# Optimization experiments

Measured on AMD Instinct MI355X. Metric: run time of the kernel, lower is better.

The kernel has to match this reference:

```python
import jax, jax.numpy as jnp
import numpy as np

B, L, D, H = 8, 512, 512, 8
E, G = 4, 2            # primary experts, ghost experts
THRESH = 0.01          # ghost_activation_threshold
EPS = 1e-5             # LayerNorm eps (torch default)


def _ln(x, s, b):
    m = x.mean(-1, keepdims=True)
    v = ((x - m) ** 2).mean(-1, keepdims=True)
    return (x - m) * jax.lax.rsqrt(v + EPS) * s + b


def _expert(x, ln1_s, ln1_b, wqkv, bqkv, wo, bo, ln2_s, ln2_b, w1, b1, w2, b2):
    # Pre-norm transformer block: MHA + residual, FFN + residual (dropout=0)
    Bn, Ln, Dn = x.shape
    dh = Dn // H
    xn = _ln(x, ln1_s, ln1_b)
    qkv = xn @ wqkv + bqkv                      # [B,L,3D]
    q, k, v = jnp.split(qkv, 3, axis=-1)
    heads = lambda t: t.reshape(Bn, Ln, H, dh).transpose(0, 2, 1, 3)
    q, k, v = heads(q), heads(k), heads(v)      # [B,H,L,dh]
    scores = jnp.einsum('bhqd,bhkd->bhqk', q, k) / np.sqrt(dh).astype(np.float32)
    attn = jax.nn.softmax(scores, axis=-1)
    o = jnp.einsum('bhqk,bhkd->bhqd', attn, v).transpose(0, 2, 1, 3).reshape(Bn, Ln, Dn)
    x = x + o @ wo + bo
    h = _ln(x, ln2_s, ln2_b)
    x = x + jax.nn.gelu(h @ w1 + b1) @ w2 + b2
    return x


def _make_params(key, n, d):
    ks = jax.random.split(key, 4)
    s = 0.02
    return dict(
        ln1_s=jnp.ones((n, d)), ln1_b=jnp.zeros((n, d)),
        wqkv=jax.random.normal(ks[0], (n, d, 3 * d)) * s, bqkv=jnp.zeros((n, 3 * d)),
        wo=jax.random.normal(ks[1], (n, d, d)) * s, bo=jnp.zeros((n, d)),
        ln2_s=jnp.ones((n, d)), ln2_b=jnp.zeros((n, d)),
        w1=jax.random.normal(ks[2], (n, d, 4 * d)) * s, b1=jnp.zeros((n, 4 * d)),
        w2=jax.random.normal(ks[3], (n, 4 * d, d)) * s, b2=jnp.zeros((n, d)))


def setup_inputs() -> dict:
    key = jax.random.key(0)
    k1, k2, k3 = jax.random.split(key, 3)
    inp = {'x': jax.random.normal(k1, (B, L, D), jnp.float32), 'step': 100}
    for pre, n, k in (('p_', E, k2), ('g_', G, k3)):
        for name, arr in _make_params(k, n, D).items():
            inp[pre + name] = arr
    return inp


def reference(x, step,
              p_ln1_s, p_ln1_b, p_wqkv, p_bqkv, p_wo, p_bo, p_ln2_s, p_ln2_b, p_w1, p_b1, p_w2, p_b2,
              g_ln1_s, g_ln1_b, g_wqkv, g_bqkv, g_wo, g_bo, g_ln2_s, g_ln2_b, g_w1, g_b1, g_w2, g_b2):
    pp = (p_ln1_s, p_ln1_b, p_wqkv, p_bqkv, p_wo, p_bo, p_ln2_s, p_ln2_b, p_w1, p_b1, p_w2, p_b2)
    gp = (g_ln1_s, g_ln1_b, g_wqkv, g_bqkv, g_wo, g_bo, g_ln2_s, g_ln2_b, g_w1, g_b1, g_w2, g_b2)
    run = jax.vmap(lambda ps: _expert(x, *ps))
    prim = run(pp)                               # [E,B,L,D]
    # --- saturation metrics (statistics only; detached like .item() in torch) ---
    mean_eo = prim.mean(axis=(1, 2))             # [E,D]
    nrm = mean_eo / jnp.linalg.norm(mean_eo, axis=1, keepdims=True)
    gram = nrm @ nrm.T                           # [E,E]
    ortho = 1.0 - jnp.mean((gram - jnp.eye(E, dtype=gram.dtype)) ** 2)
    recon = prim.mean(axis=0)                    # [B,L,D]
    uvar = jnp.var(x - recon, ddof=1)            # torch.var unbiased default
    sat = jax.lax.stop_gradient(ortho * uvar)
    # --- ghost activation (initial state: all dormant -> ghost 0 gets 0.01) ---
    base = jnp.zeros((G,), x.dtype).at[0].set(0.01)
    rates = jnp.where(sat > THRESH, base, jnp.zeros((G,), x.dtype))
    ghost = jax.vmap(lambda ps: _expert(x, *ps))(gp) * rates[:, None, None, None]  # [G,B,L,D]
    # combine: mean over all (primary + ghost) expert outputs
    out = jnp.concatenate([prim, ghost], axis=0).mean(axis=0)  # [B,L,D]
    return out
```

## Files before the change

kernel.cpp:

```cpp
#include <hip/hip_runtime.h>

typedef __bf16 bf16;
typedef __bf16 bf16x8 __attribute__((ext_vector_type(8)));
typedef float  f32x4  __attribute__((ext_vector_type(4)));
typedef float  f32x16 __attribute__((ext_vector_type(16)));

#define AS1 __attribute__((address_space(1)))
#define AS3 __attribute__((address_space(3)))

__device__ __forceinline__ void async16(const void* g, void* l) {
  __builtin_amdgcn_global_load_lds((const AS1 unsigned int*)g, (AS3 unsigned int*)l, 16, 0, 0);
}

__device__ __forceinline__ float gelu_fast(float u) {
  float z = 0.7978845608028654f * (u + 0.044715f * u * u * u);
  z = fminf(fmaxf(z, -15.f), 15.f);
  float t = __expf(2.f * z);
  return u * t / (t + 1.f);
}

template <int FOLD>
__global__ __launch_bounds__(256) void transpose_cvt(
    const float* pbase, const float* gbase, bf16* dst, int K, int M,
    const float* lnsP, const float* lnbP, const float* lnsG, const float* lnbG,
    const float* b0P, const float* b0G, float* bias_eff) {
  __shared__ float tile[32][33];
  const int z = blockIdx.z;
  const float* src = (z < 4) ? pbase + (size_t)z * K * M : gbase;
  bf16* d = dst + (size_t)z * M * K;
  const int mBlk = blockIdx.x * 32, kBlk = blockIdx.y * 32;
  const int tx = threadIdx.x, ty = threadIdx.y;
  for (int i = 0; i < 4; i++)
    tile[ty + i * 8][tx] = src[(size_t)(kBlk + ty + i * 8) * M + mBlk + tx];
  __syncthreads();
  if constexpr (FOLD) {
    const float* s  = (z < 4) ? lnsP + (size_t)z * 512 : lnsG;
    const float* bb = (z < 4) ? lnbP + (size_t)z * 512 : lnbG;
    const float sk = s[kBlk + tx];
    for (int i = 0; i < 4; i++)
      d[(size_t)(mBlk + ty + i * 8) * K + kBlk + tx] = (bf16)(tile[tx][ty + i * 8] * sk);
    if (ty == 0) {
      float acc = 0.f;
      for (int kk = 0; kk < 32; kk++) acc += bb[kBlk + kk] * tile[kk][tx];
      if (kBlk == 0) {
        const float* b0 = (z < 4) ? b0P + (size_t)z * M : b0G;
        acc += b0[mBlk + tx];
      }
      atomicAdd(&bias_eff[(size_t)z * M + mBlk + tx], acc);
    }
  } else {
    for (int i = 0; i < 4; i++)
      d[(size_t)(mBlk + ty + i * 8) * K + kBlk + tx] = (bf16)tile[tx][ty + i * 8];
  }
}

__global__ __launch_bounds__(256) void ln_plain(const float* x, bf16* out) {
  const int t = blockIdx.x, tid = threadIdx.x;
  const float* xr = x + (size_t)t * 512;
  float v0 = xr[tid], v1 = xr[tid + 256];
  float s1 = v0 + v1, s2 = v0 * v0 + v1 * v1;
  for (int off = 32; off > 0; off >>= 1) { s1 += __shfl_down(s1, off); s2 += __shfl_down(s2, off); }
  __shared__ float red[8];
  __shared__ float mv[2];
  if ((tid & 63) == 0) { red[tid >> 6] = s1; red[4 + (tid >> 6)] = s2; }
  __syncthreads();
  if (tid == 0) {
    float a = red[0] + red[1] + red[2] + red[3];
    float b = red[4] + red[5] + red[6] + red[7];
    float mean = a * (1.f / 512.f);
    float var = b * (1.f / 512.f) - mean * mean;
    mv[0] = mean; mv[1] = 1.f / sqrtf(var + 1e-5f);
  }
  __syncthreads();
  const float mean = mv[0], rs = mv[1];
  bf16* o = out + (size_t)t * 512;
  o[tid]       = (bf16)((v0 - mean) * rs);
  o[tid + 256] = (bf16)((v1 - mean) * rs);
}

__global__ __launch_bounds__(256) void ln2_kernel(const bf16* in, const float* sP, const float* bP,
                                                  const float* sG, const float* bG, bf16* out) {
  const int t = blockIdx.x, z = blockIdx.y, tid = threadIdx.x;
  const bf16* xr = in + (size_t)z * 4096 * 512 + (size_t)t * 512;
  float v0 = (float)xr[tid], v1 = (float)xr[tid + 256];
  float s1 = v0 + v1, s2 = v0 * v0 + v1 * v1;
  for (int off = 32; off > 0; off >>= 1) { s1 += __shfl_down(s1, off); s2 += __shfl_down(s2, off); }
  __shared__ float red[8];
  __shared__ float mv[2];
  if ((tid & 63) == 0) { red[tid >> 6] = s1; red[4 + (tid >> 6)] = s2; }
  __syncthreads();
  if (tid == 0) {
    float a = red[0] + red[1] + red[2] + red[3];
    float b = red[4] + red[5] + red[6] + red[7];
    float mean = a * (1.f / 512.f);
    float var = b * (1.f / 512.f) - mean * mean;
    mv[0] = mean; mv[1] = 1.f / sqrtf(var + 1e-5f);
  }
  __syncthreads();
  const float mean = mv[0], rs = mv[1];
  const float* sc = (z < 4) ? sP + (size_t)z * 512 : sG;
  const float* bi = (z < 4) ? bP + (size_t)z * 512 : bG;
  bf16* o = out + (size_t)z * 4096 * 512 + (size_t)t * 512;
  o[tid]       = (bf16)((v0 - mean) * rs * sc[tid] + bi[tid]);
  o[tid + 256] = (bf16)((v1 - mean) * rs * sc[tid + 256] + bi[tid + 256]);
}

template <int MODE>
__global__ __launch_bounds__(256, 4) void gemm_bt(
    const bf16* Abase, long long aStrideZ, const bf16* Wt,
    const float* biasP, const float* biasG, int K, int M,
    bf16* out, const void* resid, long long residStrideZ) {
  const int bx = blockIdx.x, by = blockIdx.y, z = blockIdx.z;
  const bf16* A = Abase + (size_t)z * aStrideZ;
  const bf16* B = Wt + (size_t)z * M * K;
  const float* bias = (z < 4) ? biasP + (size_t)z * M : biasG;
  __shared__ bf16 smem[128 * 136];
  bf16* As = smem;
  bf16* Bs = smem + 128 * 64;
  const int tid = threadIdx.x, wave = tid >> 6, l = tid & 63;
  const int l31 = l & 31, lh = l >> 5;
  const int wm = wave & 1, wn = wave >> 1;
  f32x16 acc[2][2];
  for (int i = 0; i < 2; i++) for (int j = 0; j < 2; j++)
    for (int r = 0; r < 16; r++) acc[i][j][r] = 0.f;
  const int rowA0 = by * 128, rowB0 = bx * 128;

  for (int kt = 0; kt < K; kt += 64) {
    __syncthreads();
    for (int i = 0; i < 4; i++) {
      int s = i * 256 + tid, r = s >> 3, kb = s & 7;
      int swz = (r ^ (r >> 3)) & 7;
      int col = kt + ((kb ^ swz) << 3);
      async16(A + (size_t)(rowA0 + r) * K + col, &As[(i * 256 + wave * 64) * 8]);
      async16(B + (size_t)(rowB0 + r) * K + col, &Bs[(i * 256 + wave * 64) * 8]);
    }
    __syncthreads();
    for (int ks = 0; ks < 4; ks++) {
      bf16x8 af[2], bfr[2];
      for (int ti = 0; ti < 2; ti++) {
        int r = wm * 64 + ti * 32 + l31;
        int kb = (ks * 2 + lh) ^ ((r ^ (r >> 3)) & 7);
        af[ti] = *(const bf16x8*)&As[r * 64 + (kb << 3)];
      }
      for (int ni = 0; ni < 2; ni++) {
        int r = wn * 64 + ni * 32 + l31;
        int kb = (ks * 2 + lh) ^ ((r ^ (r >> 3)) & 7);
        bfr[ni] = *(const bf16x8*)&Bs[r * 64 + (kb << 3)];
      }
      for (int ti = 0; ti < 2; ti++)
        for (int ni = 0; ni < 2; ni++)
          acc[ti][ni] = __builtin_amdgcn_mfma_f32_32x32x16_bf16(af[ti], bfr[ni], acc[ti][ni], 0, 0, 0);
    }
  }

  __syncthreads();
  for (int ti = 0; ti < 2; ti++)
    for (int ni = 0; ni < 2; ni++) {
      int coll = wn * 64 + ni * 32 + l31;
      float bb = bias[rowB0 + coll];
      for (int reg = 0; reg < 16; reg++) {
        int row = wm * 64 + ti * 32 + (reg & 3) + 8 * (reg >> 2) + 4 * lh;
        float v = acc[ti][ni][reg] + bb;
        if constexpr (MODE == 2) v = gelu_fast(v);
        smem[row * 136 + coll] = (bf16)v;
      }
    }
  __syncthreads();
  bf16* ob = out + (size_t)z * 4096 * M;
  for (int p = 0; p < 8; p++) {
    int r = p * 16 + (tid >> 4), c0 = (tid & 15) * 8;
    bf16x8 vv = *(const bf16x8*)&smem[r * 136 + c0];
    if constexpr (MODE == 1) {
      const float* rx = (const float*)resid + (size_t)(rowA0 + r) * 512 + rowB0 + c0;
      for (int j = 0; j < 8; j++) vv[j] = (bf16)((float)vv[j] + rx[j]);
    } else if constexpr (MODE == 3) {
      const bf16* rx = (const bf16*)resid + (size_t)z * residStrideZ + (size_t)(rowA0 + r) * 512 + rowB0 + c0;
      bf16x8 rv = *(const bf16x8*)rx;
      for (int j = 0; j < 8; j++) vv[j] = (bf16)((float)vv[j] + (float)rv[j]);
    }
    *(bf16x8*)&ob[(size_t)(rowA0 + r) * M + rowB0 + c0] = vv;
  }
}

__global__ __launch_bounds__(256, 2) void attn_kernel(const bf16* qkv, bf16* o) {
  const int qt = blockIdx.x >> 6, bh = blockIdx.x & 63, z = blockIdx.y;
  const int b = bh >> 3, h = bh & 7;
  const bf16* base = qkv + (size_t)z * 4096 * 1536 + (size_t)b * 512 * 1536;
  __shared__ bf16 smem[30208];
  bf16* Vt = smem + 16384;
  bf16* Q_area = smem + 16384;
  const int tid = threadIdx.x, wave = tid >> 6, l = tid & 63;
  const int m16 = l & 15, q4 = l >> 4;
  bf16* pw = smem + 20992 + wave * 32 * 72;
  f32x4 zero4 = {0.f, 0.f, 0.f, 0.f};

  for (int i = 0; i < 4; i++) {
    int s = i * 256 + tid, r = s >> 3, kb = s & 7;
    async16(base + (size_t)(qt * 128 + r) * 1536 + h * 64 + ((kb ^ (r & 7)) << 3),
            &Q_area[(i * 256 + wave * 64) * 8]);
  }
  for (int i = 0; i < 2; i++) {
    int s = i * 256 + tid, r = s >> 3, kb = s & 7;
    async16(base + (size_t)r * 1536 + 512 + h * 64 + ((kb ^ (r & 7)) << 3),
            &smem[(i * 256 + wave * 64) * 8]);
    async16(base + (size_t)r * 1536 + 1024 + h * 64 + (kb << 3),
            &smem[8192 + (i * 256 + wave * 64) * 8]);
  }
  f32x4 Oacc[2][4];
  float l_run[2][4];
  for (int rt = 0; rt < 2; rt++)
    for (int cr = 0; cr < 4; cr++) l_run[rt][cr] = 0.f;
  for (int rt = 0; rt < 2; rt++) for (int dt = 0; dt < 4; dt++) Oacc[rt][dt] = zero4;
  __syncthreads();
  bf16x8 qf[2][2];
  for (int rt = 0; rt < 2; rt++)
    for (int ks = 0; ks < 2; ks++) {
      int r = wave * 32 + rt * 16 + m16, kb = ks * 4 + q4;
      bf16x8 q8 = *(const bf16x8*)&Q_area[r * 64 + ((kb ^ (r & 7)) << 3)];
      for (int j = 0; j < 8; j++) q8[j] = (bf16)((float)q8[j] * 0.125f);
      qf[rt][ks] = q8;
    }
  __syncthreads();

  for (int kt = 0; kt < 8; kt++) {
    const int cur = kt & 1, nxt = cur ^ 1;
    bf16* Ks = smem + cur * 4096;
    bf16* Vs = smem + 8192 + cur * 4096;
    bf16* Ksn = smem + nxt * 4096;
    bf16* Vsn = smem + 8192 + nxt * 4096;
    if (kt > 0) __syncthreads();
    if (kt < 7) {
      for (int i = 0; i < 2; i++) {
        int s = i * 256 + tid, r = s >> 3, kb = s & 7;
        async16(base + (size_t)((kt + 1) * 64 + r) * 1536 + 512 + h * 64 + ((kb ^ (r & 7)) << 3),
                &Ksn[(i * 256 + wave * 64) * 8]);
        async16(base + (size_t)((kt + 1) * 64 + r) * 1536 + 1024 + h * 64 + (kb << 3),
                &Vsn[(i * 256 + wave * 64) * 8]);
      }
    }
    {
      int d = tid & 63, kb2 = (tid >> 6) * 16;
      for (int g = 0; g < 2; g++) {
        int kbase = kb2 + g * 8;
        bf16 tmp[8];
        for (int j = 0; j < 8; j++) tmp[j] = Vs[(kbase + j) * 64 + d];
        *(bf16x8*)&Vt[d * 72 + kbase] = *(const bf16x8*)tmp;
      }
    }
    f32x4 S[2][4];
    for (int rt = 0; rt < 2; rt++)
      for (int ct = 0; ct < 4; ct++) {
        f32x4 a = zero4;
        for (int ks = 0; ks < 2; ks++) {
          int n = ct * 16 + m16, kb = (ks * 4 + q4) ^ (n & 7);
          bf16x8 kf = *(const bf16x8*)&Ks[n * 64 + (kb << 3)];
          a = __builtin_amdgcn_mfma_f32_16x16x32_bf16(qf[rt][ks], kf, a, 0, 0, 0);
        }
        S[rt][ct] = a;
      }
    for (int rt = 0; rt < 2; rt++)
      for (int cr = 0; cr < 4; cr++) {
        float rs = 0.f;
        for (int ct = 0; ct < 4; ct++) {
          float p = __expf(S[rt][ct][cr]);
          S[rt][ct][cr] = p; rs += p;
        }
        rs += __shfl_xor(rs, 1); rs += __shfl_xor(rs, 2);
        rs += __shfl_xor(rs, 4); rs += __shfl_xor(rs, 8);
        l_run[rt][cr] += rs;
      }
    for (int rt = 0; rt < 2; rt++)
      for (int ct = 0; ct < 4; ct++)
        for (int cr = 0; cr < 4; cr++)
          pw[(rt * 16 + q4 * 4 + cr) * 72 + ct * 16 + m16] = (bf16)S[rt][ct][cr];
    __syncthreads();
    for (int rt = 0; rt < 2; rt++)
      for (int dt = 0; dt < 4; dt++) {
        f32x4 a = Oacc[rt][dt];
        for (int ks = 0; ks < 2; ks++) {
          bf16x8 pf = *(const bf16x8*)&pw[(rt * 16 + m16) * 72 + ks * 32 + q4 * 8];
          bf16x8 vf = *(const bf16x8*)&Vt[(dt * 16 + m16) * 72 + ks * 32 + q4 * 8];
          a = __builtin_amdgcn_mfma_f32_16x16x32_bf16(pf, vf, a, 0, 0, 0);
        }
        Oacc[rt][dt] = a;
      }
  }
  bf16* ob = o + (size_t)z * 4096 * 512 + (size_t)(b * 512 + qt * 128 + wave * 32) * 512 + h * 64;
  for (int rt = 0; rt < 2; rt++)
    for (int dt = 0; dt < 4; dt++)
      for (int cr = 0; cr < 4; cr++) {
        int r = rt * 16 + q4 * 4 + cr;
        ob[(size_t)r * 512 + dt * 16 + m16] = (bf16)(Oacc[rt][dt][cr] / l_run[rt][cr]);
      }
}

__global__ __launch_bounds__(256) void stats_k(const bf16* eout, const float* x,
                                               float* prim_sum, float* mean_acc, float* accum) {
  const int r0 = blockIdx.x * 32;
  const int tid = threadIdx.x;
  const int c0 = tid * 2;
  float cs[4][2] = {{0.f,0.f},{0.f,0.f},{0.f,0.f},{0.f,0.f}};
  float sd = 0.f, sd2 = 0.f;
  for (int rr = 0; rr < 32; rr++) {
    int row = r0 + rr;
    float s0 = 0.f, s1 = 0.f;
    for (int e = 0; e < 4; e++) {
      const bf16* p = &eout[((size_t)e * 4096 + row) * 512 + c0];
      float f0 = (float)p[0], f1 = (float)p[1];
      cs[e][0] += f0; cs[e][1] += f1;
      s0 += f0; s1 += f1;
    }
    prim_sum[(size_t)row * 512 + c0]     = s0;
    prim_sum[(size_t)row * 512 + c0 + 1] = s1;
    float d0 = x[(size_t)row * 512 + c0]     - s0 * 0.25f;
    float d1 = x[(size_t)row * 512 + c0 + 1] - s1 * 0.25f;
    sd += d0 + d1; sd2 += d0 * d0 + d1 * d1;
  }
  for (int e = 0; e < 4; e++) {
    atomicAdd(&mean_acc[e * 512 + c0],     cs[e][0]);
    atomicAdd(&mean_acc[e * 512 + c0 + 1], cs[e][1]);
  }
  for (int off = 32; off > 0; off >>= 1) { sd += __shfl_down(sd, off); sd2 += __shfl_down(sd2, off); }
  __shared__ float r1[4], r2[4];
  if ((tid & 63) == 0) { r1[tid >> 6] = sd; r2[tid >> 6] = sd2; }
  __syncthreads();
  if (tid == 0) {
    atomicAdd(&accum[0], r1[0] + r1[1] + r1[2] + r1[3]);
    atomicAdd(&accum[1], r2[0] + r2[1] + r2[2] + r2[3]);
  }
}

__global__ void finalize_k(const float* mean_acc, const float* accum, float* rate) {
  const int l = threadIdx.x;
  float me[4][8];
  for (int e = 0; e < 4; e++)
    for (int j = 0; j < 8; j++) me[e][j] = mean_acc[e * 512 + l * 8 + j] * (1.f / 4096.f);
  float dot[4][4];
  for (int e = 0; e < 4; e++)
    for (int f = e; f < 4; f++) {
      float d = 0.f;
      for (int j = 0; j < 8; j++) d += me[e][j] * me[f][j];
      for (int off = 32; off > 0; off >>= 1) d += __shfl_xor(d, off);
      dot[e][f] = d; dot[f][e] = d;
    }
  float nrm[4];
  for (int e = 0; e < 4; e++) nrm[e] = sqrtf(dot[e][e]);
  float acc = 0.f;
  for (int e = 0; e < 4; e++)
    for (int f = 0; f < 4; f++) {
      float g = dot[e][f] / (nrm[e] * nrm[f]) - (e == f ? 1.f : 0.f);
      acc += g * g;
    }
  float ortho = 1.f - acc * (1.f / 16.f);
  float n = 2097152.f;
  float uvar = (accum[1] - accum[0] * accum[0] / n) / (n - 1.f);
  float sat = ortho * uvar;
  if (l == 0) rate[0] = (sat > 0.01f) ? 0.01f : 0.f;
}

__global__ __launch_bounds__(256) void combine_k(const float* prim, const bf16* ghost,
                                                 const float* rate, float* out) {
  float r = rate[0];
  int i = blockIdx.x * 256 + threadIdx.x;
  f32x4 p = ((const f32x4*)prim)[i];
  const bf16* g = ghost + (size_t)i * 4;
  f32x4 o;
  for (int j = 0; j < 4; j++) o[j] = (p[j] + r * (float)g[j]) * (1.f / 6.f);
  ((f32x4*)out)[i] = o;
}

extern "C" void kernel_launch(void* const* d_in, const int* in_sizes, int n_in,
                              void* d_out, int out_size, void* d_ws, size_t ws_size,
                              hipStream_t stream) {
  const float* x       = (const float*)d_in[0];
  const float* p_ln1_s = (const float*)d_in[2];
  const float* p_ln1_b = (const float*)d_in[3];
  const float* p_wqkv  = (const float*)d_in[4];
  const float* p_bqkv  = (const float*)d_in[5];
  const float* p_wo    = (const float*)d_in[6];
  const float* p_bo    = (const float*)d_in[7];
  const float* p_ln2_s = (const float*)d_in[8];
  const float* p_ln2_b = (const float*)d_in[9];
  const float* p_w1    = (const float*)d_in[10];
  const float* p_b1    = (const float*)d_in[11];
  const float* p_w2    = (const float*)d_in[12];
  const float* p_b2    = (const float*)d_in[13];
  const float* g_ln1_s = (const float*)d_in[14];
  const float* g_ln1_b = (const float*)d_in[15];
  const float* g_wqkv  = (const float*)d_in[16];
  const float* g_bqkv  = (const float*)d_in[17];
  const float* g_wo    = (const float*)d_in[18];
  const float* g_bo    = (const float*)d_in[19];
  const float* g_ln2_s = (const float*)d_in[20];
  const float* g_ln2_b = (const float*)d_in[21];
  const float* g_w1    = (const float*)d_in[22];
  const float* g_b1    = (const float*)d_in[23];
  const float* g_w2    = (const float*)d_in[24];
  const float* g_b2    = (const float*)d_in[25];

  char* ws = (char*)d_ws;
  size_t off = 0;
  auto alloc = [&](size_t bytes) { void* p = ws + off; off += (bytes + 255) & ~(size_t)255; return p; };
  bf16* wt_qkv   = (bf16*)alloc(5ull * 1536 * 512 * 2);
  bf16* wt_wo    = (bf16*)alloc(5ull * 512 * 512 * 2);
  bf16* wt_w1    = (bf16*)alloc(5ull * 2048 * 512 * 2);
  bf16* wt_w2    = (bf16*)alloc(5ull * 512 * 2048 * 2);
  bf16* xn       = (bf16*)alloc(4096ull * 512 * 2);
  bf16* act_a    = (bf16*)alloc(5ull * 4096 * 512 * 2);
  bf16* big      = (bf16*)alloc(5ull * 4096 * 2048 * 2);
  bf16* x1       = (bf16*)alloc(5ull * 4096 * 512 * 2);
  bf16* eout     = (bf16*)alloc(5ull * 4096 * 512 * 2);
  float* prim_sum = (float*)alloc(4096ull * 512 * 4);
  float* bias_eff = (float*)alloc(5ull * 1536 * 4);
  float* mean_acc = (float*)alloc(4 * 512 * 4);
  float* accum    = (float*)alloc(256);

  (void)hipMemsetAsync(bias_eff, 0, 5ull * 1536 * 4, stream);
  (void)hipMemsetAsync(mean_acc, 0, 4 * 512 * 4, stream);
  (void)hipMemsetAsync(accum, 0, 16, stream);

  dim3 tb(32, 8);
  transpose_cvt<1><<<dim3(48, 16, 5), tb, 0, stream>>>(p_wqkv, g_wqkv, wt_qkv, 512, 1536,
      p_ln1_s, p_ln1_b, g_ln1_s, g_ln1_b, p_bqkv, g_bqkv, bias_eff);
  transpose_cvt<0><<<dim3(16, 16, 5), tb, 0, stream>>>(p_wo, g_wo, wt_wo, 512, 512,
      nullptr, nullptr, nullptr, nullptr, nullptr, nullptr, nullptr);
  transpose_cvt<0><<<dim3(64, 16, 5), tb, 0, stream>>>(p_w1, g_w1, wt_w1, 512, 2048,
      nullptr, nullptr, nullptr, nullptr, nullptr, nullptr, nullptr);
  transpose_cvt<0><<<dim3(16, 64, 5), tb, 0, stream>>>(p_w2, g_w2, wt_w2, 2048, 512,
      nullptr, nullptr, nullptr, nullptr, nullptr, nullptr, nullptr);

  ln_plain<<<dim3(4096), 256, 0, stream>>>(x, xn);
  gemm_bt<0><<<dim3(12, 32, 5), 256, 0, stream>>>(xn, 0, wt_qkv, bias_eff, bias_eff + 4ull * 1536,
                                                  512, 1536, big, nullptr, 0);
  attn_kernel<<<dim3(256, 5), 256, 0, stream>>>(big, act_a);
  gemm_bt<1><<<dim3(4, 32, 5), 256, 0, stream>>>(act_a, 4096ll * 512, wt_wo, p_bo, g_bo,
                                                 512, 512, x1, x, 0);
  ln2_kernel<<<dim3(4096, 5), 256, 0, stream>>>(x1, p_ln2_s, p_ln2_b, g_ln2_s, g_ln2_b, act_a);
  gemm_bt<2><<<dim3(16, 32, 5), 256, 0, stream>>>(act_a, 4096ll * 512, wt_w1, p_b1, g_b1,
                                                  512, 2048, big, nullptr, 0);
  gemm_bt<3><<<dim3(4, 32, 5), 256, 0, stream>>>(big, 4096ll * 2048, wt_w2, p_b2, g_b2,
                                                 2048, 512, eout, x1, 4096ll * 512);
  stats_k<<<dim3(128), 256, 0, stream>>>(eout, x, prim_sum, mean_acc, accum);
  finalize_k<<<1, 64, 0, stream>>>(mean_acc, accum, accum + 2);
  combine_k<<<dim3(2048), 256, 0, stream>>>(prim_sum, eout + 4ull * 4096 * 512, accum + 2, (float*)d_out);
}
```

Baseline: 474.1 us.

## Prefetch next GEMM K-tile into registers and group tile rasterization in bands

The GEMM main loop now loads the next K-tile from global memory into registers while MFMAs run on the current shared-memory tile, then stores it to LDS between barriers. The old version issued direct-to-LDS async loads and waited on them each iteration. Block indices are also remapped so groups of four row-tiles sweep the column tiles together, which should improve L2 reuse of the A operand. The prefetch costs extra VGPRs (32 per thread), which may hurt occupancy under launch_bounds(256,4), and it adds a register-to-LDS store step each iteration.

```diff
diff --git a/kernel.cpp b/kernel.cpp
--- a/kernel.cpp
+++ b/kernel.cpp
@@ -4,6 +4,7 @@
 typedef __bf16 bf16x8 __attribute__((ext_vector_type(8)));
 typedef float  f32x4  __attribute__((ext_vector_type(4)));
 typedef float  f32x16 __attribute__((ext_vector_type(16)));
+typedef int    i32x4  __attribute__((ext_vector_type(4)));
 
 #define AS1 __attribute__((address_space(1)))
 #define AS3 __attribute__((address_space(3)))
@@ -110,7 +111,10 @@
     const bf16* Abase, long long aStrideZ, const bf16* Wt,
     const float* biasP, const float* biasG, int K, int M,
     bf16* out, const void* resid, long long residStrideZ) {
-  const int bx = blockIdx.x, by = blockIdx.y, z = blockIdx.z;
+  const int z = blockIdx.z;
+  const int id = blockIdx.x + gridDim.x * blockIdx.y;
+  const int W = gridDim.x, band = id / (W * 4), within = id % (W * 4);
+  const int by = band * 4 + (within & 3), bx = within >> 2;
   const bf16* A = Abase + (size_t)z * aStrideZ;
   const bf16* B = Wt + (size_t)z * M * K;
   const float* bias = (z < 4) ? biasP + (size_t)z * M : biasG;
@@ -125,16 +129,35 @@
     for (int r = 0; r < 16; r++) acc[i][j][r] = 0.f;
   const int rowA0 = by * 128, rowB0 = bx * 128;
 
-  for (int kt = 0; kt < K; kt += 64) {
-    __syncthreads();
-    for (int i = 0; i < 4; i++) {
-      int s = i * 256 + tid, r = s >> 3, kb = s & 7;
-      int swz = (r ^ (r >> 3)) & 7;
-      int col = kt + ((kb ^ swz) << 3);
-      async16(A + (size_t)(rowA0 + r) * K + col, &As[(i * 256 + wave * 64) * 8]);
-      async16(B + (size_t)(rowB0 + r) * K + col, &Bs[(i * 256 + wave * 64) * 8]);
-    }
-    __syncthreads();
+  const int s0 = tid, r0 = s0 >> 3, kb0 = s0 & 7;
+  const int swzc = ((r0 ^ (r0 >> 3)) & 7);
+  const int colsw = (kb0 ^ swzc) << 3;
+  const bf16* ap[4];
+  const bf16* bp[4];
+  for (int i = 0; i < 4; i++) {
+    int r = i * 32 + r0;
+    int sw = ((r ^ (r >> 3)) & 7);
+    int cs = (kb0 ^ sw) << 3;
+    ap[i] = A + (size_t)(rowA0 + r) * K + cs;
+    bp[i] = B + (size_t)(rowB0 + r) * K + cs;
+  }
+
+  for (int i = 0; i < 4; i++) {
+    async16(ap[i], &As[(i * 256 + wave * 64) * 8]);
+    async16(bp[i], &Bs[(i * 256 + wave * 64) * 8]);
+  }
+  __syncthreads();
+
+  const int nk = K >> 6;
+  i32x4 sa[4], sb[4];
+  for (int kt = 0; kt < nk; kt++) {
+    if (kt + 1 < nk) {
+      int coff = (kt + 1) * 64;
+      for (int i = 0; i < 4; i++) {
+        sa[i] = *(const i32x4*)(ap[i] + coff);
+        sb[i] = *(const i32x4*)(bp[i] + coff);
+      }
+    }
     for (int ks = 0; ks < 4; ks++) {
       bf16x8 af[2], bfr[2];
       for (int ti = 0; ti < 2; ti++) {
@@ -150,6 +173,14 @@
       for (int ti = 0; ti < 2; ti++)
         for (int ni = 0; ni < 2; ni++)
           acc[ti][ni] = __builtin_amdgcn_mfma_f32_32x32x16_bf16(af[ti], bfr[ni], acc[ti][ni], 0, 0, 0);
+    }
+    if (kt + 1 < nk) {
+      __syncthreads();
+      for (int i = 0; i < 4; i++) {
+        *(i32x4*)&As[(i * 256 + tid) * 8] = sa[i];
+        *(i32x4*)&Bs[(i * 256 + tid) * 8] = sb[i];
+      }
+      __syncthreads();
     }
   }
 
```

Measured after the change: 544.7 us. 14.9% more time.

## Enlarge GEMM tiles to 256x128 with band-swizzled block order

Applied to the files above, without the earlier changes.

The bf16 GEMM tile grows from 128x128 to 256x128, so each wave holds 4x2 MFMA accumulators, and the grid is halved in the row dimension. Block IDs are remapped into bands of four row tiles so that neighbouring blocks share weight tiles in cache. The epilogue now stages output in two 128-row halves through shared memory. The aim is more MFMA work per LDS load and less repeated global traffic, at the cost of more registers (launch bounds drop from 4 to 2 blocks per CU), fewer blocks in flight, and one extra barrier in the epilogue.

```diff
diff --git a/kernel.cpp b/kernel.cpp
--- a/kernel.cpp
+++ b/kernel.cpp
@@ -106,39 +106,45 @@
 }
 
 template <int MODE>
-__global__ __launch_bounds__(256, 4) void gemm_bt(
+__global__ __launch_bounds__(256, 2) void gemm_bt(
     const bf16* Abase, long long aStrideZ, const bf16* Wt,
     const float* biasP, const float* biasG, int K, int M,
     bf16* out, const void* resid, long long residStrideZ) {
-  const int bx = blockIdx.x, by = blockIdx.y, z = blockIdx.z;
+  const int z = blockIdx.z;
+  const int id = blockIdx.x + gridDim.x * blockIdx.y;
+  const int W = gridDim.x, band = id / (W * 4), within = id % (W * 4);
+  const int by = band * 4 + (within & 3), bx = within >> 2;
   const bf16* A = Abase + (size_t)z * aStrideZ;
   const bf16* B = Wt + (size_t)z * M * K;
   const float* bias = (z < 4) ? biasP + (size_t)z * M : biasG;
-  __shared__ bf16 smem[128 * 136];
+  __shared__ bf16 smem[24576];
   bf16* As = smem;
-  bf16* Bs = smem + 128 * 64;
+  bf16* Bs = smem + 16384;
   const int tid = threadIdx.x, wave = tid >> 6, l = tid & 63;
   const int l31 = l & 31, lh = l >> 5;
   const int wm = wave & 1, wn = wave >> 1;
-  f32x16 acc[2][2];
-  for (int i = 0; i < 2; i++) for (int j = 0; j < 2; j++)
+  f32x16 acc[4][2];
+  for (int i = 0; i < 4; i++) for (int j = 0; j < 2; j++)
     for (int r = 0; r < 16; r++) acc[i][j][r] = 0.f;
-  const int rowA0 = by * 128, rowB0 = bx * 128;
+  const int rowA0 = by * 256, rowB0 = bx * 128;
 
   for (int kt = 0; kt < K; kt += 64) {
     __syncthreads();
+    for (int i = 0; i < 8; i++) {
+      int s = i * 256 + tid, r = s >> 3, kb = s & 7;
+      int col = kt + ((kb ^ ((r ^ (r >> 3)) & 7)) << 3);
+      async16(A + (size_t)(rowA0 + r) * K + col, &As[(i * 256 + wave * 64) * 8]);
+    }
     for (int i = 0; i < 4; i++) {
       int s = i * 256 + tid, r = s >> 3, kb = s & 7;
-      int swz = (r ^ (r >> 3)) & 7;
-      int col = kt + ((kb ^ swz) << 3);
-      async16(A + (size_t)(rowA0 + r) * K + col, &As[(i * 256 + wave * 64) * 8]);
+      int col = kt + ((kb ^ ((r ^ (r >> 3)) & 7)) << 3);
       async16(B + (size_t)(rowB0 + r) * K + col, &Bs[(i * 256 + wave * 64) * 8]);
     }
     __syncthreads();
     for (int ks = 0; ks < 4; ks++) {
-      bf16x8 af[2], bfr[2];
-      for (int ti = 0; ti < 2; ti++) {
-        int r = wm * 64 + ti * 32 + l31;
+      bf16x8 af[4], bfr[2];
+      for (int ti = 0; ti < 4; ti++) {
+        int r = wm * 128 + ti * 32 + l31;
         int kb = (ks * 2 + lh) ^ ((r ^ (r >> 3)) & 7);
         af[ti] = *(const bf16x8*)&As[r * 64 + (kb << 3)];
       }
@@ -147,38 +153,44 @@
         int kb = (ks * 2 + lh) ^ ((r ^ (r >> 3)) & 7);
         bfr[ni] = *(const bf16x8*)&Bs[r * 64 + (kb << 3)];
       }
-      for (int ti = 0; ti < 2; ti++)
+      for (int ti = 0; ti < 4; ti++)
         for (int ni = 0; ni < 2; ni++)
           acc[ti][ni] = __builtin_amdgcn_mfma_f32_32x32x16_bf16(af[ti], bfr[ni], acc[ti][ni], 0, 0, 0);
     }
   }
 
   __syncthreads();
-  for (int ti = 0; ti < 2; ti++)
-    for (int ni = 0; ni < 2; ni++) {
-      int coll = wn * 64 + ni * 32 + l31;
-      float bb = bias[rowB0 + coll];
-      for (int reg = 0; reg < 16; reg++) {
-        int row = wm * 64 + ti * 32 + (reg & 3) + 8 * (reg >> 2) + 4 * lh;
-        float v = acc[ti][ni][reg] + bb;
-        if constexpr (MODE == 2) v = gelu_fast(v);
-        smem[row * 136 + coll] = (bf16)v;
-      }
-    }
-  __syncthreads();
   bf16* ob = out + (size_t)z * 4096 * M;
-  for (int p = 0; p < 8; p++) {
-    int r = p * 16 + (tid >> 4), c0 = (tid & 15) * 8;
-    bf16x8 vv = *(const bf16x8*)&smem[r * 136 + c0];
-    if constexpr (MODE == 1) {
-      const float* rx = (const float*)resid + (size_t)(rowA0 + r) * 512 + rowB0 + c0;
-      for (int j = 0; j < 8; j++) vv[j] = (bf16)((float)vv[j] + rx[j]);
-    } else if constexpr (MODE == 3) {
-      const bf16* rx = (const bf16*)resid + (size_t)z * residStrideZ + (size_t)(rowA0 + r) * 512 + rowB0 + c0;
-      bf16x8 rv = *(const bf16x8*)rx;
-      for (int j = 0; j < 8; j++) vv[j] = (bf16)((float)vv[j] + (float)rv[j]);
-    }
-    *(bf16x8*)&ob[(size_t)(rowA0 + r) * M + rowB0 + c0] = vv;
+  for (int p2 = 0; p2 < 2; p2++) {
+    if (wm == p2) {
+      for (int ti = 0; ti < 4; ti++)
+        for (int ni = 0; ni < 2; ni++) {
+          int coll = wn * 64 + ni * 32 + l31;
+          float bb = bias[rowB0 + coll];
+          for (int reg = 0; reg < 16; reg++) {
+            int row = ti * 32 + (reg & 3) + 8 * (reg >> 2) + 4 * lh;
+            float v = acc[ti][ni][reg] + bb;
+            if constexpr (MODE == 2) v = gelu_fast(v);
+            smem[row * 136 + coll] = (bf16)v;
+          }
+        }
+    }
+    __syncthreads();
+    for (int p = 0; p < 8; p++) {
+      int r = p * 16 + (tid >> 4), c0 = (tid & 15) * 8;
+      int grow = rowA0 + p2 * 128 + r;
+      bf16x8 vv = *(const bf16x8*)&smem[r * 136 + c0];
+      if constexpr (MODE == 1) {
+        const float* rx = (const float*)resid + (size_t)grow * 512 + rowB0 + c0;
+        for (int j = 0; j < 8; j++) vv[j] = (bf16)((float)vv[j] + rx[j]);
+      } else if constexpr (MODE == 3) {
+        const bf16* rx = (const bf16*)resid + (size_t)z * residStrideZ + (size_t)grow * 512 + rowB0 + c0;
+        bf16x8 rv = *(const bf16x8*)rx;
+        for (int j = 0; j < 8; j++) vv[j] = (bf16)((float)vv[j] + (float)rv[j]);
+      }
+      *(bf16x8*)&ob[(size_t)grow * M + rowB0 + c0] = vv;
+    }
+    if (p2 == 0) __syncthreads();
   }
 }
 
@@ -430,15 +442,15 @@
       nullptr, nullptr, nullptr, nullptr, nullptr, nullptr, nullptr);
 
   ln_plain<<<dim3(4096), 256, 0, stream>>>(x, xn);
-  gemm_bt<0><<<dim3(12, 32, 5), 256, 0, stream>>>(xn, 0, wt_qkv, bias_eff, bias_eff + 4ull * 1536,
+  gemm_bt<0><<<dim3(12, 16, 5), 256, 0, stream>>>(xn, 0, wt_qkv, bias_eff, bias_eff + 4ull * 1536,
                                                   512, 1536, big, nullptr, 0);
   attn_kernel<<<dim3(256, 5), 256, 0, stream>>>(big, act_a);
-  gemm_bt<1><<<dim3(4, 32, 5), 256, 0, stream>>>(act_a, 4096ll * 512, wt_wo, p_bo, g_bo,
+  gemm_bt<1><<<dim3(4, 16, 5), 256, 0, stream>>>(act_a, 4096ll * 512, wt_wo, p_bo, g_bo,
                                                  512, 512, x1, x, 0);
   ln2_kernel<<<dim3(4096, 5), 256, 0, stream>>>(x1, p_ln2_s, p_ln2_b, g_ln2_s, g_ln2_b, act_a);
-  gemm_bt<2><<<dim3(16, 32, 5), 256, 0, stream>>>(act_a, 4096ll * 512, wt_w1, p_b1, g_b1,
+  gemm_bt<2><<<dim3(16, 16, 5), 256, 0, stream>>>(act_a, 4096ll * 512, wt_w1, p_b1, g_b1,
                                                   512, 2048, big, nullptr, 0);
-  gemm_bt<3><<<dim3(4, 32, 5), 256, 0, stream>>>(big, 4096ll * 2048, wt_w2, p_b2, g_b2,
+  gemm_bt<3><<<dim3(4, 16, 5), 256, 0, stream>>>(big, 4096ll * 2048, wt_w2, p_b2, g_b2,
                                                  2048, 512, eout, x1, 4096ll * 512);
   stats_k<<<dim3(128), 256, 0, stream>>>(eout, x, prim_sum, mean_acc, accum);
   finalize_k<<<1, 64, 0, stream>>>(mean_acc, accum, accum + 2);
```

After: 578.5 us. 1.22x slower.
